# Kernel optimization log

Hardware: AMD Instinct MI355X
Metric: run time of the kernel (lower is better)

The kernel has to match this reference:

```python
import jax, jax.numpy as jnp
import numpy as np

NOPE, ROPE, VDIM, QKD = 128, 64, 128, 192
H = 16
EPS = 1e-6
SCALING = QKD ** -0.5


def rms_norm(x, w):
    xf = x.astype(jnp.float32)
    var = jnp.mean(xf * xf, axis=-1, keepdims=True)
    return (w * (xf * jax.lax.rsqrt(var + EPS))).astype(x.dtype)


def rotate_half(x):
    d = x.shape[-1] // 2
    return jnp.concatenate((-x[..., d:], x[..., :d]), axis=-1)


def apply_rope(q, k, cos, sin):
    # cos/sin: [B,S,D] -> unsqueeze head dim
    cos = cos[:, None, :, :]
    sin = sin[:, None, :, :]
    return q * cos + rotate_half(q) * sin, k * cos + rotate_half(k) * sin


def setup_inputs() -> dict:
    key = jax.random.key(0)
    ks = jax.random.split(key, 8)
    B, S, D = 2, 2048, 2048
    pos = jnp.arange(S, dtype=jnp.float32)
    inv_freq = 1.0 / (10000.0 ** (jnp.arange(0, ROPE, 2, dtype=jnp.float32) / ROPE))
    ang = pos[:, None] * inv_freq[None, :]            # [S, ROPE/2]
    emb = jnp.concatenate([ang, ang], axis=-1)        # [S, ROPE]
    cos = jnp.broadcast_to(jnp.cos(emb)[None], (B, S, ROPE))
    sin = jnp.broadcast_to(jnp.sin(emb)[None], (B, S, ROPE))
    s = lambda k, shp, fan: jax.random.normal(k, shp, jnp.float32) * (fan ** -0.5)
    return {
        "hidden_states": jax.random.normal(ks[0], (B, S, D), jnp.float32),
        "cos": cos,
        "sin": sin,
        "q_a_W": s(ks[1], (1536, D), D),
        "q_a_norm_w": jnp.ones((1536,), jnp.float32),
        "q_b_W": s(ks[2], (H * QKD, 1536), 1536),
        "kv_a_W": s(ks[3], (512 + ROPE, D), D),
        "kv_a_norm_w": jnp.ones((512,), jnp.float32),
        "kv_b_W": s(ks[4], (H * (NOPE + VDIM), 512), 512),
        "o_W": s(ks[5], (D, H * VDIM), H * VDIM),
    }


def reference(hidden_states, cos, sin, q_a_W, q_a_norm_w, q_b_W, kv_a_W,
              kv_a_norm_w, kv_b_W, o_W):
    B, S, D = hidden_states.shape
    # low-rank Q path
    q = rms_norm(hidden_states @ q_a_W.T, q_a_norm_w) @ q_b_W.T   # [B,S,H*QKD]
    q = q.reshape(B, S, H, QKD).transpose(0, 2, 1, 3)             # [B,H,S,QKD]
    q_pass, q_rot = q[..., :NOPE], q[..., NOPE:]
    # compressed KV path
    ckv = hidden_states @ kv_a_W.T                                # [B,S,512+ROPE]
    k_lat, k_rot = ckv[..., :512], ckv[..., 512:]
    kv = rms_norm(k_lat, kv_a_norm_w) @ kv_b_W.T                  # [B,S,H*(NOPE+VDIM)]
    kv = kv.reshape(B, S, H, NOPE + VDIM).transpose(0, 2, 1, 3)   # [B,H,S,*]
    k_pass, v = kv[..., :NOPE], kv[..., NOPE:]
    k_rot = k_rot.reshape(B, 1, S, ROPE)
    q_rot, k_rot = apply_rope(q_rot, k_rot, cos, sin)
    k_rot = jnp.broadcast_to(k_rot, (B, H, S, ROPE))
    query = jnp.concatenate((q_pass, q_rot), axis=-1)             # [B,H,S,QKD]
    key = jnp.concatenate((k_pass, k_rot), axis=-1)
    # eager causal attention
    scores = jnp.einsum('bhsd,bhtd->bhst', query, key) * SCALING
    causal = jnp.tril(jnp.ones((S, S), bool))
    scores = jnp.where(causal, scores, jnp.finfo(scores.dtype).min)
    attn = jax.nn.softmax(scores.astype(jnp.float32), axis=-1).astype(query.dtype)
    out = jnp.einsum('bhst,bhtd->bhsd', attn, v)                  # [B,H,S,VDIM]
    out = out.transpose(0, 2, 1, 3).reshape(B, S, H * VDIM)
    return out @ o_W.T
```

## Files before the change

kernel.cpp:

```cpp
#include <hip/hip_runtime.h>
#include <hip/hip_bf16.h>


typedef __bf16 bf16x8 __attribute__((ext_vector_type(8)));
typedef float floatx4 __attribute__((ext_vector_type(4)));
#define BF16 __hip_bfloat16

static __device__ __forceinline__ BF16 f2b(float x) { return __float2bfloat16(x); }

static __device__ __forceinline__ void load_lds16(const BF16* g, BF16* l) {
  __builtin_amdgcn_global_load_lds((__attribute__((address_space(1))) void*)(void*)g,
                                   (__attribute__((address_space(3))) void*)(void*)l,
                                   16, 0, 0);
}

struct CastArgs {
  const float* src[6];
  BF16* dst[6];
  long n[6];
};
__global__ void cast_multi_k(CastArgs a) {
  int r = blockIdx.y;
  long n = a.n[r];
  const float* __restrict__ x = a.src[r];
  BF16* __restrict__ y = a.dst[r];
  for (long i = ((long)blockIdx.x * 256 + threadIdx.x) * 4; i + 3 < n;
       i += (long)gridDim.x * 1024) {
    float4 v = *(const float4*)(x + i);
    y[i+0] = f2b(v.x); y[i+1] = f2b(v.y); y[i+2] = f2b(v.z); y[i+3] = f2b(v.w);
  }
}

template<int OUT_MODE>
__global__ __launch_bounds__(256) void gemm_lds(const BF16* __restrict__ A, const BF16* __restrict__ B,
                                                void* __restrict__ C, int M, int N, int K,
                                                const float* __restrict__ cosb,
                                                const float* __restrict__ sinb,
                                                BF16* __restrict__ P1, BF16* __restrict__ P2) {
  __shared__ __align__(16) BF16 As[128*32];
  __shared__ __align__(16) BF16 Bs[128*32];
  int tid = threadIdx.x, wave = tid >> 6, lane = tid & 63;
  int wr = wave >> 1, wc = wave & 1, lr = lane & 15, quad = lane >> 4;
  long m0 = (long)blockIdx.y * 128, n0 = (long)blockIdx.x * 128;

  int c0 = wave*64 + lane, c1 = c0 + 256;
  const BF16* ga0 = A + (m0 + (c0>>2))*(long)K + (c0&3)*8;
  const BF16* ga1 = A + (m0 + (c1>>2))*(long)K + (c1&3)*8;
  long bn0 = n0 + (c0>>2); if (bn0 >= N) bn0 = N-1;
  long bn1 = n0 + (c1>>2); if (bn1 >= N) bn1 = N-1;
  const BF16* gb0 = B + bn0*(long)K + (c0&3)*8;
  const BF16* gb1 = B + bn1*(long)K + (c1&3)*8;
  BF16* la0 = As + wave*512;
  BF16* la1 = As + wave*512 + 2048;
  BF16* lb0 = Bs + wave*512;
  BF16* lb1 = Bs + wave*512 + 2048;

  floatx4 acc[4][4] = {};
  for (int k0 = 0; k0 < K; k0 += 32) {
    __syncthreads();
    load_lds16(ga0 + k0, la0);
    load_lds16(ga1 + k0, la1);
    load_lds16(gb0 + k0, lb0);
    load_lds16(gb1 + k0, lb1);
    __syncthreads();
    bf16x8 a[4], b[4];
#pragma unroll
    for (int i = 0; i < 4; i++) a[i] = *(const bf16x8*)(As + (wr*64 + i*16 + lr)*32 + quad*8);
#pragma unroll
    for (int j = 0; j < 4; j++) b[j] = *(const bf16x8*)(Bs + (wc*64 + j*16 + lr)*32 + quad*8);
#pragma unroll
    for (int i = 0; i < 4; i++)
#pragma unroll
      for (int j = 0; j < 4; j++)
        acc[i][j] = __builtin_amdgcn_mfma_f32_16x16x32_bf16(a[i], b[j], acc[i][j], 0, 0, 0);
  }

  long n0w = n0 + wc*64;
  const float SCALE = 0.07216878364870322f;
#pragma unroll
  for (int i = 0; i < 4; i++) {
#pragma unroll
    for (int r = 0; r < 4; r++) {
      long row = m0 + wr*64 + i*16 + quad*4 + r;
      long b = row >> 11, s = row & 2047;
      if (OUT_MODE == 0) {
#pragma unroll
        for (int j = 0; j < 4; j++) {
          long col = n0w + j*16 + lr;
          if (col < N) ((float*)C)[row*(long)N + col] = acc[i][j][r];
        }
      } else if (OUT_MODE == 2) {
#pragma unroll
        for (int j = 0; j < 4; j++) {
          long col = n0w + j*16 + lr;
          long h = col >> 8, d = col & 255;
          long base = (b*16 + h)*2048 + s;
          if (d < 128) P1[base*192 + d] = f2b(acc[i][j][r]);
          else         P2[base*128 + d - 128] = f2b(acc[i][j][r]);
        }
      } else {
        bool rope = ((n0w % 192) == 128);
#pragma unroll
        for (int j = 0; j < 4; j++) {
          long col = n0w + j*16 + lr;
          float x = acc[i][j][r], val;
          if (rope) {
            int id = j*16 + lr;
            float partner = acc[i][j^2][r];
            float rot = (j < 2) ? -partner : partner;
            val = x*cosb[row*64 + id] + rot*sinb[row*64 + id];
          } else {
            val = x;
          }
          long h = col / 192, d = col % 192;
          P1[((b*16 + h)*2048 + s)*192 + d] = f2b(val * SCALE);
        }
      }
    }
  }
}

template<int D>
__global__ __launch_bounds__(256) void rmsnorm_k(const float* __restrict__ x, const float* __restrict__ w,
                                                 BF16* __restrict__ y, int ld_in, int ld_out) {
  long row = blockIdx.x;
  const float* xr = x + row * (long)ld_in;
  float ss = 0.f;
  for (int i = threadIdx.x * 4; i < D; i += 1024) {
    float4 v = *(const float4*)(xr + i);
    ss += v.x*v.x + v.y*v.y + v.z*v.z + v.w*v.w;
  }
#pragma unroll
  for (int off = 32; off > 0; off >>= 1) ss += __shfl_down(ss, off);
  __shared__ float red[4];
  if ((threadIdx.x & 63) == 0) red[threadIdx.x >> 6] = ss;
  __syncthreads();
  float tot = red[0] + red[1] + red[2] + red[3];
  float rs = rsqrtf(tot / (float)D + 1e-6f);
  BF16* yr = y + row * (long)ld_out;
  for (int i = threadIdx.x * 4; i < D; i += 1024) {
    float4 v = *(const float4*)(xr + i);
    yr[i+0] = f2b(v.x * w[i+0] * rs);
    yr[i+1] = f2b(v.y * w[i+1] * rs);
    yr[i+2] = f2b(v.z * w[i+2] * rs);
    yr[i+3] = f2b(v.w * w[i+3] * rs);
  }
}

__global__ void prep_krot_k(const float* __restrict__ krot, int ld, const float* __restrict__ cosb,
                            const float* __restrict__ sinb, BF16* __restrict__ Kt) {
  long row = blockIdx.x; int i = threadIdx.x;
  const float* kr = krot + row * (long)ld;
  float x = kr[i];
  float rot = (i < 32) ? -kr[i + 32] : kr[i - 32];
  BF16 v = f2b(x * cosb[row*64 + i] + rot * sinb[row*64 + i]);
  long b = row >> 11, s = row & 2047;
  long base = ((b*16)*2048 + s)*192 + 128 + i;
#pragma unroll
  for (int h = 0; h < 16; h++) Kt[base + (long)h*2048*192] = v;
}

#define LK 200
#define LV 72
#define LP 72
__global__ __launch_bounds__(256) void flash_k(const BF16* __restrict__ Qt, const BF16* __restrict__ Kt,
                                               const BF16* __restrict__ Vt, BF16* __restrict__ O) {
  __shared__ __align__(16) BF16 Ks[64*LK];
  __shared__ __align__(16) BF16 Vs[128*LV];
  __shared__ __align__(16) BF16 Ps[4][16*LP];
  int tid = threadIdx.x, wave = tid >> 6, lane = tid & 63;
  int lr = lane & 15, quad = lane >> 4;
  int F = blockIdx.x;
  int g = F & 31, jidx = F >> 5;
  int h = g & 15, b = g >> 4;
  const BF16* Qb = Qt + ((long)(b*16 + h) * 2048) * 192;
  const BF16* Kb = Kt + ((long)(b*16 + h) * 2048) * 192;
  const BF16* Vb = Vt + ((long)(b*16 + h) * 2048) * 128;
  const float NEG_INF = -__builtin_inff();

  int krow[6], kcol[6];
#pragma unroll
  for (int i = 0; i < 6; i++) {
    int c = tid + 256*i;
    krow[i] = c / 24; kcol[i] = (c % 24) * 8;
  }
  int vd0base = wave * 8;

  bf16x8 kreg[6], vreg[4];
  auto stage_load = [&](int k0) {
#pragma unroll
    for (int i = 0; i < 6; i++)
      kreg[i] = *(const bf16x8*)(Kb + (long)(k0 + krow[i])*192 + kcol[i]);
#pragma unroll
    for (int it = 0; it < 4; it++)
      vreg[it] = *(const bf16x8*)(Vb + (long)(k0 + lane)*128 + vd0base + it*32);
  };
  auto stage_store = [&]() {
#pragma unroll
    for (int i = 0; i < 6; i++)
      *(bf16x8*)(Ks + krow[i]*LK + kcol[i]) = kreg[i];
#pragma unroll
    for (int it = 0; it < 4; it++) {
      int vd0 = vd0base + it*32;
#pragma unroll
      for (int j = 0; j < 8; j++) Vs[(vd0+j)*LV + lane] = ((BF16*)&vreg[it])[j];
    }
  };

  for (int half = 0; half < 2; half++) {
    int qt = (half == 0) ? jidx : 31 - jidx;
    int q0 = qt * 64;
    bf16x8 qf[6];
    {
      const BF16* qp = Qb + (long)(q0 + wave*16 + lr) * 192 + quad*8;
#pragma unroll
      for (int f = 0; f < 6; f++) qf[f] = *(const bf16x8*)(qp + f*32);
    }
    float m_i[4], l_i[4];
#pragma unroll
    for (int r = 0; r < 4; r++) { m_i[r] = NEG_INF; l_i[r] = 0.f; }
    floatx4 o_acc[8] = {};
    int nk = qt + 1;
    stage_load(0);
    for (int kt = 0; kt < nk; kt++) {
      int k0 = kt * 64;
      __syncthreads();
      stage_store();
      __syncthreads();
      if (kt + 1 < nk) stage_load(k0 + 64);
      floatx4 st[4];
#pragma unroll
      for (int t = 0; t < 4; t++) {
        floatx4 c = {};
#pragma unroll
        for (int f = 0; f < 6; f++) {
          bf16x8 kf = *(const bf16x8*)(Ks + (t*16+lr)*LK + f*32 + quad*8);
          c = __builtin_amdgcn_mfma_f32_16x16x32_bf16(qf[f], kf, c, 0, 0, 0);
        }
        st[t] = c;
      }
      int rowbase = q0 + wave*16 + quad*4;
      float mt[4];
#pragma unroll
      for (int r = 0; r < 4; r++) mt[r] = NEG_INF;
      if (kt == qt) {
#pragma unroll
        for (int t = 0; t < 4; t++) {
          int col = k0 + t*16 + lr;
#pragma unroll
          for (int r = 0; r < 4; r++) {
            float s = st[t][r];
            if (col > rowbase + r) s = NEG_INF;
            st[t][r] = s;
            mt[r] = fmaxf(mt[r], s);
          }
        }
      } else {
#pragma unroll
        for (int t = 0; t < 4; t++)
#pragma unroll
          for (int r = 0; r < 4; r++) mt[r] = fmaxf(mt[r], st[t][r]);
      }
#pragma unroll
      for (int off = 1; off < 16; off <<= 1)
#pragma unroll
        for (int r = 0; r < 4; r++) mt[r] = fmaxf(mt[r], __shfl_xor(mt[r], off));
      float alpha[4], rsum[4];
#pragma unroll
      for (int r = 0; r < 4; r++) {
        float mn = fmaxf(m_i[r], mt[r]);
        alpha[r] = __expf(m_i[r] - mn);
        m_i[r] = mn;
        rsum[r] = 0.f;
      }
#pragma unroll
      for (int t = 0; t < 4; t++)
#pragma unroll
        for (int r = 0; r < 4; r++) {
          float p = __expf(st[t][r] - m_i[r]);
          st[t][r] = p;
          rsum[r] += p;
        }
#pragma unroll
      for (int off = 1; off < 16; off <<= 1)
#pragma unroll
        for (int r = 0; r < 4; r++) rsum[r] += __shfl_xor(rsum[r], off);
#pragma unroll
      for (int r = 0; r < 4; r++) l_i[r] = l_i[r]*alpha[r] + rsum[r];
#pragma unroll
      for (int v = 0; v < 8; v++)
#pragma unroll
        for (int r = 0; r < 4; r++) o_acc[v][r] *= alpha[r];
#pragma unroll
      for (int t = 0; t < 4; t++)
#pragma unroll
        for (int r = 0; r < 4; r++)
          Ps[wave][(quad*4 + r)*LP + t*16 + lr] = f2b(st[t][r]);
#pragma unroll
      for (int kc = 0; kc < 2; kc++) {
        bf16x8 pa = *(const bf16x8*)(&Ps[wave][lr*LP + kc*32 + quad*8]);
#pragma unroll
        for (int v = 0; v < 8; v++) {
          bf16x8 vf = *(const bf16x8*)(&Vs[(v*16+lr)*LV + kc*32 + quad*8]);
          o_acc[v] = __builtin_amdgcn_mfma_f32_16x16x32_bf16(pa, vf, o_acc[v], 0, 0, 0);
        }
      }
    }
    long rowb = q0 + wave*16 + quad*4;
#pragma unroll
    for (int v = 0; v < 8; v++)
#pragma unroll
      for (int r = 0; r < 4; r++) {
        long row = rowb + r;
        O[((long)b*2048 + row)*2048 + h*128 + v*16 + lr] = f2b(o_acc[v][r] / l_i[r]);
      }
  }
}

extern "C" void kernel_launch(void* const* d_in, const int* in_sizes, int n_in,
                              void* d_out, int out_size, void* d_ws, size_t ws_size,
                              hipStream_t stream) {
  const float* hidden      = (const float*)d_in[0];
  const float* cosb        = (const float*)d_in[1];
  const float* sinb        = (const float*)d_in[2];
  const float* q_a_W       = (const float*)d_in[3];
  const float* q_a_norm_w  = (const float*)d_in[4];
  const float* q_b_W       = (const float*)d_in[5];
  const float* kv_a_W      = (const float*)d_in[6];
  const float* kv_a_norm_w = (const float*)d_in[7];
  const float* kv_b_W      = (const float*)d_in[8];
  const float* o_W         = (const float*)d_in[9];
  float* out = (float*)d_out;

  const int Mrows = 4096;

  char* ws = (char*)d_ws; size_t off = 0;
  auto alloc = [&](size_t bytes) -> void* {
    void* p = ws + off; off = (off + bytes + 255) & ~(size_t)255; return p;
  };
  BF16* hb    = (BF16*)alloc((size_t)4096*2048*2);
  BF16* Wqakv = (BF16*)alloc((size_t)2112*2048*2);
  BF16* Wqb   = (BF16*)alloc((size_t)3072*1536*2);
  BF16* Wkvb  = (BF16*)alloc((size_t)4096*512*2);
  BF16* Wo    = (BF16*)alloc((size_t)2048*2048*2);
  float* qakv = (float*)alloc((size_t)4096*2112*4);
  BF16* qan   = (BF16*)alloc((size_t)4096*1536*2);
  BF16* kvn   = (BF16*)alloc((size_t)4096*512*2);
  BF16* Qt    = (BF16*)alloc((size_t)2*16*2048*192*2);
  BF16* Kt    = (BF16*)alloc((size_t)2*16*2048*192*2);
  BF16* Vt    = (BF16*)alloc((size_t)2*16*2048*128*2);
  BF16* attn  = (BF16*)alloc((size_t)4096*2048*2);

  CastArgs ca;
  ca.src[0] = hidden;  ca.dst[0] = hb;                 ca.n[0] = (long)4096*2048;
  ca.src[1] = q_a_W;   ca.dst[1] = Wqakv;              ca.n[1] = (long)1536*2048;
  ca.src[2] = kv_a_W;  ca.dst[2] = Wqakv + (long)1536*2048; ca.n[2] = (long)576*2048;
  ca.src[3] = q_b_W;   ca.dst[3] = Wqb;                ca.n[3] = (long)3072*1536;
  ca.src[4] = kv_b_W;  ca.dst[4] = Wkvb;               ca.n[4] = (long)4096*512;
  ca.src[5] = o_W;     ca.dst[5] = Wo;                 ca.n[5] = (long)2048*2048;
  cast_multi_k<<<dim3(1024, 6), dim3(256), 0, stream>>>(ca);

  gemm_lds<0><<<dim3(17, 32), dim3(256), 0, stream>>>(hb, Wqakv, qakv, Mrows, 2112, 2048,
                                                      nullptr, nullptr, nullptr, nullptr);
  rmsnorm_k<1536><<<dim3(4096), dim3(256), 0, stream>>>(qakv, q_a_norm_w, qan, 2112, 1536);
  rmsnorm_k<512><<<dim3(4096), dim3(256), 0, stream>>>(qakv + 1536, kv_a_norm_w, kvn, 2112, 512);
  prep_krot_k<<<dim3(4096), dim3(64), 0, stream>>>(qakv + 2048, 2112, cosb, sinb, Kt);

  gemm_lds<3><<<dim3(24, 32), dim3(256), 0, stream>>>(qan, Wqb, nullptr, Mrows, 3072, 1536,
                                                      cosb, sinb, Qt, nullptr);
  gemm_lds<2><<<dim3(32, 32), dim3(256), 0, stream>>>(kvn, Wkvb, nullptr, Mrows, 4096, 512,
                                                      nullptr, nullptr, Kt, Vt);

  flash_k<<<dim3(512), dim3(256), 0, stream>>>(Qt, Kt, Vt, attn);

  gemm_lds<0><<<dim3(16, 32), dim3(256), 0, stream>>>(attn, Wo, out, Mrows, 2048, 2048,
                                                      nullptr, nullptr, nullptr, nullptr);
}
```

Measured before the change: 504.1 us.

## Process 128-row query tiles per block sharing K/V loads, pre-transposed V, exp2 softmax

The flash kernel now handles two adjacent 64-row query sub-tiles per block, so each staged K/V tile serves both, where before a block took two separate mirrored 64-row tiles. The kv_b GEMM epilogue writes V already transposed ([B,H,D,S]) with packed 4-element stores, so the flash kernel loads V into LDS with vectorized copies and no per-element transpose. The Q scaling now folds in log2(e) so the softmax can use the hardware exp2 instruction, and launch bounds request 2 blocks per CU. In exchange, registers per thread roughly double for the Q fragments and accumulators. Blocks also become unequal in work (later tiles do more), replacing the previous mirrored pairing that balanced the causal load.

```diff
diff --git a/kernel.cpp b/kernel.cpp
--- a/kernel.cpp
+++ b/kernel.cpp
@@ -7,6 +7,8 @@
 #define BF16 __hip_bfloat16
 
 static __device__ __forceinline__ BF16 f2b(float x) { return __float2bfloat16(x); }
+static __device__ __forceinline__ unsigned short b2u(BF16 x) { return *(unsigned short*)&x; }
+static __device__ __forceinline__ float fast_exp2(float x) { return __builtin_amdgcn_exp2f(x); }
 
 static __device__ __forceinline__ void load_lds16(const BF16* g, BF16* l) {
   __builtin_amdgcn_global_load_lds((__attribute__((address_space(1))) void*)(void*)g,
@@ -76,30 +78,42 @@
   }
 
   long n0w = n0 + wc*64;
-  const float SCALE = 0.07216878364870322f;
+  const float SCALE_L2E = 0.104117546f;
 #pragma unroll
   for (int i = 0; i < 4; i++) {
-#pragma unroll
-    for (int r = 0; r < 4; r++) {
-      long row = m0 + wr*64 + i*16 + quad*4 + r;
-      long b = row >> 11, s = row & 2047;
-      if (OUT_MODE == 0) {
+    long tok = m0 + wr*64 + i*16 + quad*4;
+    long bb = tok >> 11, s = tok & 2047;
+    if (OUT_MODE == 0) {
+#pragma unroll
+      for (int r = 0; r < 4; r++) {
+        long row = tok + r;
 #pragma unroll
         for (int j = 0; j < 4; j++) {
           long col = n0w + j*16 + lr;
           if (col < N) ((float*)C)[row*(long)N + col] = acc[i][j][r];
         }
-      } else if (OUT_MODE == 2) {
-#pragma unroll
-        for (int j = 0; j < 4; j++) {
-          long col = n0w + j*16 + lr;
-          long h = col >> 8, d = col & 255;
-          long base = (b*16 + h)*2048 + s;
-          if (d < 128) P1[base*192 + d] = f2b(acc[i][j][r]);
-          else         P2[base*128 + d - 128] = f2b(acc[i][j][r]);
-        }
-      } else {
-        bool rope = ((n0w % 192) == 128);
+      }
+    } else if (OUT_MODE == 2) {
+#pragma unroll
+      for (int j = 0; j < 4; j++) {
+        long col = n0w + j*16 + lr;
+        long h = col >> 8, d = col & 255;
+        if (d < 128) {
+#pragma unroll
+          for (int r = 0; r < 4; r++)
+            P1[((bb*16 + h)*2048 + s + r)*192 + d] = f2b(acc[i][j][r]);
+        } else {
+          ushort4 pk;
+          pk.x = b2u(f2b(acc[i][j][0])); pk.y = b2u(f2b(acc[i][j][1]));
+          pk.z = b2u(f2b(acc[i][j][2])); pk.w = b2u(f2b(acc[i][j][3]));
+          *(ushort4*)(P2 + ((bb*16 + h)*128 + d - 128)*2048 + s) = pk;
+        }
+      }
+    } else {
+      bool rope = ((n0w % 192) == 128);
+#pragma unroll
+      for (int r = 0; r < 4; r++) {
+        long row = tok + r;
 #pragma unroll
         for (int j = 0; j < 4; j++) {
           long col = n0w + j*16 + lr;
@@ -113,7 +127,7 @@
             val = x;
           }
           long h = col / 192, d = col % 192;
-          P1[((b*16 + h)*2048 + s)*192 + d] = f2b(val * SCALE);
+          P1[((bb*16 + h)*2048 + s + r)*192 + d] = f2b(val * SCALE_L2E);
         }
       }
     }
@@ -163,20 +177,21 @@
 #define LK 200
 #define LV 72
 #define LP 72
-__global__ __launch_bounds__(256) void flash_k(const BF16* __restrict__ Qt, const BF16* __restrict__ Kt,
-                                               const BF16* __restrict__ Vt, BF16* __restrict__ O) {
+__global__ __launch_bounds__(256, 2) void flash_k(const BF16* __restrict__ Qt, const BF16* __restrict__ Kt,
+                                                  const BF16* __restrict__ Vt, BF16* __restrict__ O) {
   __shared__ __align__(16) BF16 Ks[64*LK];
   __shared__ __align__(16) BF16 Vs[128*LV];
   __shared__ __align__(16) BF16 Ps[4][16*LP];
   int tid = threadIdx.x, wave = tid >> 6, lane = tid & 63;
   int lr = lane & 15, quad = lane >> 4;
   int F = blockIdx.x;
-  int g = F & 31, jidx = F >> 5;
+  int g = F & 31, qti = 15 - (F >> 5);
   int h = g & 15, b = g >> 4;
   const BF16* Qb = Qt + ((long)(b*16 + h) * 2048) * 192;
   const BF16* Kb = Kt + ((long)(b*16 + h) * 2048) * 192;
-  const BF16* Vb = Vt + ((long)(b*16 + h) * 2048) * 128;
+  const BF16* Vb = Vt + ((long)(b*16 + h) * 128) * 2048;
   const float NEG_INF = -__builtin_inff();
+  int q0 = qti * 128;
 
   int krow[6], kcol[6];
 #pragma unroll
@@ -184,7 +199,12 @@
     int c = tid + 256*i;
     krow[i] = c / 24; kcol[i] = (c % 24) * 8;
   }
-  int vd0base = wave * 8;
+  int vrow[4], vcol[4];
+#pragma unroll
+  for (int i = 0; i < 4; i++) {
+    int c = tid + 256*i;
+    vrow[i] = c >> 3; vcol[i] = (c & 7) * 8;
+  }
 
   bf16x8 kreg[6], vreg[4];
   auto stage_load = [&](int k0) {
@@ -192,42 +212,44 @@
     for (int i = 0; i < 6; i++)
       kreg[i] = *(const bf16x8*)(Kb + (long)(k0 + krow[i])*192 + kcol[i]);
 #pragma unroll
-    for (int it = 0; it < 4; it++)
-      vreg[it] = *(const bf16x8*)(Vb + (long)(k0 + lane)*128 + vd0base + it*32);
+    for (int i = 0; i < 4; i++)
+      vreg[i] = *(const bf16x8*)(Vb + (long)vrow[i]*2048 + k0 + vcol[i]);
   };
   auto stage_store = [&]() {
 #pragma unroll
     for (int i = 0; i < 6; i++)
       *(bf16x8*)(Ks + krow[i]*LK + kcol[i]) = kreg[i];
 #pragma unroll
-    for (int it = 0; it < 4; it++) {
-      int vd0 = vd0base + it*32;
-#pragma unroll
-      for (int j = 0; j < 8; j++) Vs[(vd0+j)*LV + lane] = ((BF16*)&vreg[it])[j];
-    }
+    for (int i = 0; i < 4; i++)
+      *(bf16x8*)(Vs + vrow[i]*LV + vcol[i]) = vreg[i];
   };
 
-  for (int half = 0; half < 2; half++) {
-    int qt = (half == 0) ? jidx : 31 - jidx;
-    int q0 = qt * 64;
-    bf16x8 qf[6];
-    {
-      const BF16* qp = Qb + (long)(q0 + wave*16 + lr) * 192 + quad*8;
-#pragma unroll
-      for (int f = 0; f < 6; f++) qf[f] = *(const bf16x8*)(qp + f*32);
-    }
-    float m_i[4], l_i[4];
-#pragma unroll
-    for (int r = 0; r < 4; r++) { m_i[r] = NEG_INF; l_i[r] = 0.f; }
-    floatx4 o_acc[8] = {};
-    int nk = qt + 1;
-    stage_load(0);
-    for (int kt = 0; kt < nk; kt++) {
-      int k0 = kt * 64;
-      __syncthreads();
-      stage_store();
-      __syncthreads();
-      if (kt + 1 < nk) stage_load(k0 + 64);
+  bf16x8 qf[2][6];
+#pragma unroll
+  for (int s = 0; s < 2; s++) {
+    const BF16* qp = Qb + (long)(q0 + s*64 + wave*16 + lr) * 192 + quad*8;
+#pragma unroll
+    for (int f = 0; f < 6; f++) qf[s][f] = *(const bf16x8*)(qp + f*32);
+  }
+  float m_i[2][4], l_i[2][4];
+#pragma unroll
+  for (int s = 0; s < 2; s++)
+#pragma unroll
+    for (int r = 0; r < 4; r++) { m_i[s][r] = NEG_INF; l_i[s][r] = 0.f; }
+  floatx4 o_acc[2][8] = {};
+
+  int nk = 2*qti + 2;
+  stage_load(0);
+  for (int kt = 0; kt < nk; kt++) {
+    int k0 = kt * 64;
+    __syncthreads();
+    stage_store();
+    __syncthreads();
+    if (kt + 1 < nk) stage_load(k0 + 64);
+#pragma unroll
+    for (int s = 0; s < 2; s++) {
+      int diag = 2*qti + s;
+      if (kt > diag) continue;
       floatx4 st[4];
 #pragma unroll
       for (int t = 0; t < 4; t++) {
@@ -235,24 +257,23 @@
 #pragma unroll
         for (int f = 0; f < 6; f++) {
           bf16x8 kf = *(const bf16x8*)(Ks + (t*16+lr)*LK + f*32 + quad*8);
-          c = __builtin_amdgcn_mfma_f32_16x16x32_bf16(qf[f], kf, c, 0, 0, 0);
+          c = __builtin_amdgcn_mfma_f32_16x16x32_bf16(qf[s][f], kf, c, 0, 0, 0);
         }
         st[t] = c;
       }
-      int rowbase = q0 + wave*16 + quad*4;
       float mt[4];
 #pragma unroll
       for (int r = 0; r < 4; r++) mt[r] = NEG_INF;
-      if (kt == qt) {
+      if (kt == diag) {
 #pragma unroll
         for (int t = 0; t < 4; t++) {
-          int col = k0 + t*16 + lr;
+          int coff = t*16 + lr;
 #pragma unroll
           for (int r = 0; r < 4; r++) {
-            float s = st[t][r];
-            if (col > rowbase + r) s = NEG_INF;
-            st[t][r] = s;
-            mt[r] = fmaxf(mt[r], s);
+            float sc = st[t][r];
+            if (coff > wave*16 + quad*4 + r) sc = NEG_INF;
+            st[t][r] = sc;
+            mt[r] = fmaxf(mt[r], sc);
           }
         }
       } else {
@@ -268,16 +289,16 @@
       float alpha[4], rsum[4];
 #pragma unroll
       for (int r = 0; r < 4; r++) {
-        float mn = fmaxf(m_i[r], mt[r]);
-        alpha[r] = __expf(m_i[r] - mn);
-        m_i[r] = mn;
+        float mn = fmaxf(m_i[s][r], mt[r]);
+        alpha[r] = fast_exp2(m_i[s][r] - mn);
+        m_i[s][r] = mn;
         rsum[r] = 0.f;
       }
 #pragma unroll
       for (int t = 0; t < 4; t++)
 #pragma unroll
         for (int r = 0; r < 4; r++) {
-          float p = __expf(st[t][r] - m_i[r]);
+          float p = fast_exp2(st[t][r] - m_i[s][r]);
           st[t][r] = p;
           rsum[r] += p;
         }
@@ -286,11 +307,11 @@
 #pragma unroll
         for (int r = 0; r < 4; r++) rsum[r] += __shfl_xor(rsum[r], off);
 #pragma unroll
-      for (int r = 0; r < 4; r++) l_i[r] = l_i[r]*alpha[r] + rsum[r];
+      for (int r = 0; r < 4; r++) l_i[s][r] = l_i[s][r]*alpha[r] + rsum[r];
 #pragma unroll
       for (int v = 0; v < 8; v++)
 #pragma unroll
-        for (int r = 0; r < 4; r++) o_acc[v][r] *= alpha[r];
+        for (int r = 0; r < 4; r++) o_acc[s][v][r] *= alpha[r];
 #pragma unroll
       for (int t = 0; t < 4; t++)
 #pragma unroll
@@ -302,17 +323,20 @@
 #pragma unroll
         for (int v = 0; v < 8; v++) {
           bf16x8 vf = *(const bf16x8*)(&Vs[(v*16+lr)*LV + kc*32 + quad*8]);
-          o_acc[v] = __builtin_amdgcn_mfma_f32_16x16x32_bf16(pa, vf, o_acc[v], 0, 0, 0);
+          o_acc[s][v] = __builtin_amdgcn_mfma_f32_16x16x32_bf16(pa, vf, o_acc[s][v], 0, 0, 0);
         }
       }
     }
-    long rowb = q0 + wave*16 + quad*4;
+  }
+#pragma unroll
+  for (int s = 0; s < 2; s++) {
+    long rowb = q0 + s*64 + wave*16 + quad*4;
 #pragma unroll
     for (int v = 0; v < 8; v++)
 #pragma unroll
       for (int r = 0; r < 4; r++) {
         long row = rowb + r;
-        O[((long)b*2048 + row)*2048 + h*128 + v*16 + lr] = f2b(o_acc[v][r] / l_i[r]);
+        O[((long)b*2048 + row)*2048 + h*128 + v*16 + lr] = f2b(o_acc[s][v][r] / l_i[s][r]);
       }
   }
 }
@@ -348,7 +372,7 @@
   BF16* kvn   = (BF16*)alloc((size_t)4096*512*2);
   BF16* Qt    = (BF16*)alloc((size_t)2*16*2048*192*2);
   BF16* Kt    = (BF16*)alloc((size_t)2*16*2048*192*2);
-  BF16* Vt    = (BF16*)alloc((size_t)2*16*2048*128*2);
+  BF16* Vt    = (BF16*)alloc((size_t)2*16*128*2048*2);
   BF16* attn  = (BF16*)alloc((size_t)4096*2048*2);
 
   CastArgs ca;
```

After: 543.4 us. +7.8%, slower.
